# Kernel tuning notes

Hardware: AMD Instinct MI355X
Metric: run time of the kernel (lower is better)

## Reference

```python
import jax, jax.numpy as jnp
import numpy as np
from jax import lax

B, P = 32, 1024          # batch, max_phonemes
V, E, H = 100, 512, 512  # vocab, embedding_dim, hidden_dim
EPS = 1e-5


def setup_inputs() -> dict:
    key = jax.random.key(0)
    ks = jax.random.split(key, 12)
    return {
        "phoneme_ids": jax.random.randint(ks[0], (B, P), 0, V),
        "phoneme_durations": jax.random.randint(ks[1], (B, P), 0, 10),
        "emb": jax.random.normal(ks[2], (V, E), jnp.float32) * 0.02,
        "conv1_w": jax.random.normal(ks[3], (H, E, 3), jnp.float32) * 0.02,
        "conv1_b": jnp.zeros((H,), jnp.float32),
        "bn1_gamma": 1.0 + 0.1 * jax.random.normal(ks[4], (H,), jnp.float32),
        "bn1_beta": 0.1 * jax.random.normal(ks[5], (H,), jnp.float32),
        "bn1_mean": jnp.zeros((H,), jnp.float32),
        "bn1_var": jnp.ones((H,), jnp.float32),
        "conv2_w": jax.random.normal(ks[6], (H, H, 3), jnp.float32) * 0.02,
        "conv2_b": jnp.zeros((H,), jnp.float32),
        "bn2_gamma": 1.0 + 0.1 * jax.random.normal(ks[7], (H,), jnp.float32),
        "bn2_beta": 0.1 * jax.random.normal(ks[8], (H,), jnp.float32),
        "bn2_mean": jnp.zeros((H,), jnp.float32),
        "bn2_var": jnp.ones((H,), jnp.float32),
    }


def _conv_bn_relu(x, w, b, gamma, beta, mean, var):
    # x: [B, C, P]; w: [O, C, 3]; 'same' padding conv1d, inference batchnorm, relu
    y = lax.conv_general_dilated(x, w, (1,), [(1, 1)],
                                 dimension_numbers=("NCH", "OIH", "NCH"))
    y = y + b[None, :, None]
    scale = gamma * lax.rsqrt(var + EPS)
    y = y * scale[None, :, None] + (beta - mean * scale)[None, :, None]
    return jax.nn.relu(y)


def _upsample(x, durations):
    # x: [B, H, P], durations: [B, P] int -> [B, H, max_frames]
    cum = jnp.cumsum(durations, axis=1)              # [B, P]
    total = cum[:, -1]                               # [B]
    max_frames = int(jnp.max(total))                 # concrete (data-derived shape)
    frames = jnp.arange(max_frames)                  # [F]
    # frame f belongs to phoneme p iff cum[p-1] <= f < cum[p]
    idx = jax.vmap(lambda c: jnp.searchsorted(c, frames, side="right"))(cum)
    idx = jnp.minimum(idx, P - 1)                    # [B, F]
    gathered = jnp.take_along_axis(x, idx[:, None, :], axis=2)  # [B, H, F]
    mask = (frames[None, :] < total[:, None]).astype(x.dtype)   # [B, F]
    return gathered * mask[:, None, :]


def reference(phoneme_ids, phoneme_durations, emb,
              conv1_w, conv1_b, bn1_gamma, bn1_beta, bn1_mean, bn1_var,
              conv2_w, conv2_b, bn2_gamma, bn2_beta, bn2_mean, bn2_var):
    x = emb[phoneme_ids]                 # [B, P, E]
    x = jnp.transpose(x, (0, 2, 1))      # [B, E, P]
    x = _conv_bn_relu(x, conv1_w, conv1_b, bn1_gamma, bn1_beta, bn1_mean, bn1_var)
    x = _conv_bn_relu(x, conv2_w, conv2_b, bn2_gamma, bn2_beta, bn2_mean, bn2_var)
    return _upsample(x, phoneme_durations)
```

## Files before the change

### kernel.cpp

```cpp
#include <hip/hip_runtime.h>

#define B_ 32
#define P_ 1024
#define V_ 100
#define E_ 512
#define H_ 512
#define C_ 512
#define EPS_ 1e-5f

typedef float f32x4 __attribute__((ext_vector_type(4)));
typedef short bf16x8 __attribute__((ext_vector_type(8)));

#define GLB(p) ((const __attribute__((address_space(1))) unsigned int*)(p))
#define LDSP(p) ((__attribute__((address_space(3))) unsigned int*)(p))

__device__ __forceinline__ unsigned short f2bf(float f) {
  unsigned int u = __float_as_uint(f);
  u += 0x7fffu + ((u >> 16) & 1u);
  return (unsigned short)(u >> 16);
}
__device__ __forceinline__ float bf2f(unsigned short s) {
  return __uint_as_float(((unsigned int)s) << 16);
}

__global__ void g_kernel(const float* __restrict__ emb, const float* __restrict__ w1,
                         const float* __restrict__ g1, const float* __restrict__ vr1,
                         float* __restrict__ G) {
  __shared__ float se[E_];
  int v = blockIdx.x;
  int h = threadIdx.x;
  se[h] = emb[(size_t)v * E_ + h];
  __syncthreads();
  float a0 = 0.f, a1 = 0.f, a2 = 0.f;
  const float* wrow = w1 + (size_t)h * E_ * 3;
#pragma unroll 4
  for (int e = 0; e < E_; ++e) {
    float x = se[e];
    a0 = fmaf(wrow[e * 3 + 0], x, a0);
    a1 = fmaf(wrow[e * 3 + 1], x, a1);
    a2 = fmaf(wrow[e * 3 + 2], x, a2);
  }
  float sc = g1[h] * rsqrtf(vr1[h] + EPS_);
  G[((size_t)0 * V_ + v) * H_ + h] = a0 * sc;
  G[((size_t)1 * V_ + v) * H_ + h] = a1 * sc;
  G[((size_t)2 * V_ + v) * H_ + h] = a2 * sc;
}

__global__ void a2_kernel(const float* __restrict__ w2,
                          const float* __restrict__ b1, const float* __restrict__ g1,
                          const float* __restrict__ be1, const float* __restrict__ mn1,
                          const float* __restrict__ vr1,
                          const float* __restrict__ b2, const float* __restrict__ g2,
                          const float* __restrict__ be2, const float* __restrict__ mn2,
                          const float* __restrict__ vr2,
                          float* __restrict__ bias1, float* __restrict__ bias2,
                          unsigned short* __restrict__ A2h, unsigned short* __restrict__ A2l) {
  int h = blockIdx.x;
  int tid = threadIdx.x;
  float sc1 = g1[h] * rsqrtf(vr1[h] + EPS_);
  float sc2 = g2[h] * rsqrtf(vr2[h] + EPS_);
  if (tid == 0) {
    bias1[h] = b1[h] * sc1 + be1[h] - mn1[h] * sc1;
    bias2[h] = b2[h] * sc2 + be2[h] - mn2[h] * sc2;
  }
  for (int j = tid; j < 3 * C_; j += 256) {
    int k = j >> 9;
    int c = j & (C_ - 1);
    float val = w2[((size_t)h * C_ + c) * 3 + k] * sc2;
    unsigned short hi = f2bf(val);
    A2h[(size_t)h * (3 * C_) + j] = hi;
    A2l[(size_t)h * (3 * C_) + j] = f2bf(val - bf2f(hi));
  }
}

__global__ void embed_conv1_kernel(const int* __restrict__ ids, const float* __restrict__ G,
                                   const float* __restrict__ bias1,
                                   unsigned short* __restrict__ Bh, unsigned short* __restrict__ Bl) {
  int r = blockIdx.x % (P_ + 2);
  int b = blockIdx.x / (P_ + 2);
  int tid = threadIdx.x;
  size_t outbase = ((size_t)b * (P_ + 2) + r) * C_;
  if (r == 0 || r == P_ + 1) {
    for (int c = tid; c < C_; c += 256) { Bh[outbase + c] = 0; Bl[outbase + c] = 0; }
    return;
  }
  int p = r - 1;
  int v0 = (p >= 1) ? ids[b * P_ + p - 1] : -1;
  int v1 = ids[b * P_ + p];
  int v2 = (p + 1 < P_) ? ids[b * P_ + p + 1] : -1;
  const float* G0 = (v0 >= 0) ? (G + ((size_t)0 * V_ + v0) * H_) : nullptr;
  const float* G1 = G + ((size_t)1 * V_ + v1) * H_;
  const float* G2 = (v2 >= 0) ? (G + ((size_t)2 * V_ + v2) * H_) : nullptr;
  for (int c = tid; c < C_; c += 256) {
    float s = bias1[c] + G1[c];
    if (G0) s += G0[c];
    if (G2) s += G2[c];
    s = fmaxf(s, 0.f);
    unsigned short hi = f2bf(s);
    Bh[outbase + c] = hi;
    Bl[outbase + c] = f2bf(s - bf2f(hi));
  }
}

__global__ void cumsum_kernel(const int* __restrict__ dur, int* __restrict__ cum) {
  __shared__ int s[P_];
  int b = blockIdx.x;
  int t = threadIdx.x;
  s[t] = dur[b * P_ + t];
  __syncthreads();
  for (int off = 1; off < P_; off <<= 1) {
    int v = (t >= off) ? s[t - off] : 0;
    __syncthreads();
    s[t] += v;
    __syncthreads();
  }
  cum[b * P_ + t] = s[t];
}

#define BM 128
#define BN 128
#define BK 32
__global__ __launch_bounds__(256) void conv2_gemm_kernel(
    const unsigned short* __restrict__ A2h, const unsigned short* __restrict__ A2l,
    const unsigned short* __restrict__ Bh, const unsigned short* __restrict__ Bl,
    const float* __restrict__ bias2, float* __restrict__ out2) {
  __shared__ __align__(16) unsigned short lds[4][BM * BK];

  int tid = threadIdx.x;
  int w = tid >> 6;
  int l = tid & 63;
  int m0 = blockIdx.y * BM;
  int n0 = blockIdx.x * BN;
  int b = n0 >> 10;
  int p0 = n0 & (P_ - 1);

  const unsigned short* Ah_base = A2h + (size_t)m0 * (3 * C_);
  const unsigned short* Al_base = A2l + (size_t)m0 * (3 * C_);
  const unsigned short* Bh_base = Bh + ((size_t)b * (P_ + 2) + p0) * C_;
  const unsigned short* Bl_base = Bl + ((size_t)b * (P_ + 2) + p0) * C_;

  f32x4 acc[4][4] = {};

  int srow = l >> 2;
  int scol = (l & 3) * 8;
  int fr = l & 15, fq = l >> 4;
  int wr = (w >> 1) * 64, wc = (w & 1) * 64;

  for (int kt = 0; kt < (3 * C_) / BK; ++kt) {
    int kofs = kt * BK;
#pragma unroll
    for (int q = 0; q < 2; ++q) {
      int seg = q * 4 + w;
      int row = seg * 16 + srow;
      int col = kofs + scol;
      __builtin_amdgcn_global_load_lds(GLB(Ah_base + (size_t)row * (3 * C_) + col),
                                       LDSP(&lds[0][seg * 512]), 16, 0, 0);
      __builtin_amdgcn_global_load_lds(GLB(Al_base + (size_t)row * (3 * C_) + col),
                                       LDSP(&lds[1][seg * 512]), 16, 0, 0);
      __builtin_amdgcn_global_load_lds(GLB(Bh_base + (size_t)row * C_ + col),
                                       LDSP(&lds[2][seg * 512]), 16, 0, 0);
      __builtin_amdgcn_global_load_lds(GLB(Bl_base + (size_t)row * C_ + col),
                                       LDSP(&lds[3][seg * 512]), 16, 0, 0);
    }
    __syncthreads();

    bf16x8 ah[4], al[4], bh[4], bl[4];
#pragma unroll
    for (int i = 0; i < 4; ++i) {
      ah[i] = *(const bf16x8*)&lds[0][(wr + i * 16 + fr) * BK + fq * 8];
      al[i] = *(const bf16x8*)&lds[1][(wr + i * 16 + fr) * BK + fq * 8];
    }
#pragma unroll
    for (int j = 0; j < 4; ++j) {
      bh[j] = *(const bf16x8*)&lds[2][(wc + j * 16 + fr) * BK + fq * 8];
      bl[j] = *(const bf16x8*)&lds[3][(wc + j * 16 + fr) * BK + fq * 8];
    }
#pragma unroll
    for (int i = 0; i < 4; ++i)
#pragma unroll
      for (int j = 0; j < 4; ++j) {
        acc[i][j] = __builtin_amdgcn_mfma_f32_16x16x32_bf16(ah[i], bh[j], acc[i][j], 0, 0, 0);
        acc[i][j] = __builtin_amdgcn_mfma_f32_16x16x32_bf16(ah[i], bl[j], acc[i][j], 0, 0, 0);
        acc[i][j] = __builtin_amdgcn_mfma_f32_16x16x32_bf16(al[i], bh[j], acc[i][j], 0, 0, 0);
      }
    __syncthreads();
  }

#pragma unroll
  for (int i = 0; i < 4; ++i) {
#pragma unroll
    for (int j = 0; j < 4; ++j) {
#pragma unroll
      for (int r = 0; r < 4; ++r) {
        int m = m0 + wr + i * 16 + fq * 4 + r;
        int n = n0 + wc + j * 16 + fr;
        int bb = n >> 10;
        int p = n & (P_ - 1);
        float v = acc[i][j][r] + bias2[m];
        v = fmaxf(v, 0.f);
        out2[((size_t)bb * H_ + m) * P_ + p] = v;
      }
    }
  }
}

__global__ void upsample_kernel(const float* __restrict__ out2, const int* __restrict__ cum,
                                float* __restrict__ out, int T) {
  __shared__ int sc[P_];
  int b = blockIdx.y;
  int tid = threadIdx.x;
  for (int i = tid; i < P_; i += 256) sc[i] = cum[b * P_ + i];
  __syncthreads();
  int t = blockIdx.x * 256 + tid;
  if (t >= T) return;
  int tot = sc[P_ - 1];
  bool valid = (t < tot);
  int idx = 0;
  if (valid) {
    int lo = 0, hi = P_;
    while (lo < hi) {
      int mid = (lo + hi) >> 1;
      if (sc[mid] <= t) lo = mid + 1; else hi = mid;
    }
    idx = min(lo, P_ - 1);
  }
  const float* src = out2 + (size_t)b * H_ * P_ + idx;
  float* dst = out + (size_t)b * H_ * T + t;
  if (valid) {
    for (int h = 0; h < H_; ++h) dst[(size_t)h * T] = src[(size_t)h * P_];
  } else {
    for (int h = 0; h < H_; ++h) dst[(size_t)h * T] = 0.f;
  }
}

static inline size_t align256(size_t x) { return (x + 255) & ~(size_t)255; }

extern "C" void kernel_launch(void* const* d_in, const int* in_sizes, int n_in,
                              void* d_out, int out_size, void* d_ws, size_t ws_size,
                              hipStream_t stream) {
  const int*   ids = (const int*)d_in[0];
  const int*   dur = (const int*)d_in[1];
  const float* emb = (const float*)d_in[2];
  const float* w1  = (const float*)d_in[3];
  const float* b1  = (const float*)d_in[4];
  const float* g1  = (const float*)d_in[5];
  const float* be1 = (const float*)d_in[6];
  const float* mn1 = (const float*)d_in[7];
  const float* vr1 = (const float*)d_in[8];
  const float* w2  = (const float*)d_in[9];
  const float* b2  = (const float*)d_in[10];
  const float* g2  = (const float*)d_in[11];
  const float* be2 = (const float*)d_in[12];
  const float* mn2 = (const float*)d_in[13];
  const float* vr2 = (const float*)d_in[14];
  float* out = (float*)d_out;

  int T = out_size / (B_ * H_);

  char* ws = (char*)d_ws;
  size_t off = 0;
  auto carve = [&](size_t bytes) { void* p = ws + off; off = align256(off + bytes); return p; };
  float* G              = (float*)carve((size_t)3 * V_ * H_ * 4);
  float* bias1          = (float*)carve(H_ * 4);
  float* bias2          = (float*)carve(H_ * 4);
  unsigned short* A2h   = (unsigned short*)carve((size_t)H_ * 3 * C_ * 2);
  unsigned short* A2l   = (unsigned short*)carve((size_t)H_ * 3 * C_ * 2);
  unsigned short* Bhv   = (unsigned short*)carve((size_t)B_ * (P_ + 2) * C_ * 2);
  unsigned short* Blv   = (unsigned short*)carve((size_t)B_ * (P_ + 2) * C_ * 2);
  float* out2           = (float*)carve((size_t)B_ * H_ * P_ * 4);
  int* cum              = (int*)carve((size_t)B_ * P_ * 4);

  g_kernel<<<V_, E_, 0, stream>>>(emb, w1, g1, vr1, G);
  a2_kernel<<<H_, 256, 0, stream>>>(w2, b1, g1, be1, mn1, vr1, b2, g2, be2, mn2, vr2,
                                    bias1, bias2, A2h, A2l);
  embed_conv1_kernel<<<B_ * (P_ + 2), 256, 0, stream>>>(ids, G, bias1, Bhv, Blv);
  cumsum_kernel<<<B_, P_, 0, stream>>>(dur, cum);
  conv2_gemm_kernel<<<dim3((B_ * P_) / BN, H_ / BM), 256, 0, stream>>>(A2h, A2l, Bhv, Blv,
                                                                       bias2, out2);
  upsample_kernel<<<dim3((T + 255) / 256, B_), 256, 0, stream>>>(out2, cum, out, T);
}
```

Baseline: 744.3 us.

## Transpose conv1 weights, vectorize embed stores, remap GEMM block order

Adds a tiled transpose of conv1 weights so g_kernel reads coalesced rows, and splits g_kernel across more blocks of 64 threads. embed_conv1 now uses float2 loads and packed 32-bit bf16 stores. The conv2 GEMM grid is flattened and remapped with a swizzle across groups of 8 blocks to change L2 locality. Several launch bounds are added. The costs are an extra kernel launch and a 3 MB workspace buffer.

```diff
diff --git a/kernel.cpp b/kernel.cpp
--- a/kernel.cpp
+++ b/kernel.cpp
@@ -23,22 +23,40 @@
   return __uint_as_float(((unsigned int)s) << 16);
 }
 
-__global__ void g_kernel(const float* __restrict__ emb, const float* __restrict__ w1,
-                         const float* __restrict__ g1, const float* __restrict__ vr1,
-                         float* __restrict__ G) {
+__global__ __launch_bounds__(256) void w1t_kernel(const float* __restrict__ w1,
+                                                  float* __restrict__ w1T) {
+  __shared__ float tile[64][65];
+  int h0 = blockIdx.x * 64;
+  int e0 = blockIdx.y * 64;
+  int t = threadIdx.x;
+  int c = t & 63, r4 = t >> 6;
+#pragma unroll
+  for (int r = 0; r < 64; r += 4)
+    tile[r + r4][c] = w1[(size_t)(h0 + r + r4) * 1536 + e0 + c];
+  __syncthreads();
+#pragma unroll
+  for (int r = 0; r < 64; r += 4)
+    w1T[(size_t)(e0 + r + r4) * 512 + h0 + c] = tile[c][r + r4];
+}
+
+__global__ __launch_bounds__(64) void g_kernel(const float* __restrict__ emb,
+                                               const float* __restrict__ w1T,
+                                               const float* __restrict__ g1,
+                                               const float* __restrict__ vr1,
+                                               float* __restrict__ G) {
   __shared__ float se[E_];
   int v = blockIdx.x;
-  int h = threadIdx.x;
-  se[h] = emb[(size_t)v * E_ + h];
+  int h = blockIdx.y * 64 + threadIdx.x;
+  for (int i = threadIdx.x; i < E_; i += 64) se[i] = emb[(size_t)v * E_ + i];
   __syncthreads();
   float a0 = 0.f, a1 = 0.f, a2 = 0.f;
-  const float* wrow = w1 + (size_t)h * E_ * 3;
 #pragma unroll 4
   for (int e = 0; e < E_; ++e) {
     float x = se[e];
-    a0 = fmaf(wrow[e * 3 + 0], x, a0);
-    a1 = fmaf(wrow[e * 3 + 1], x, a1);
-    a2 = fmaf(wrow[e * 3 + 2], x, a2);
+    const float* wp = w1T + (size_t)(3 * e) * H_ + h;
+    a0 = fmaf(wp[0], x, a0);
+    a1 = fmaf(wp[H_], x, a1);
+    a2 = fmaf(wp[2 * H_], x, a2);
   }
   float sc = g1[h] * rsqrtf(vr1[h] + EPS_);
   G[((size_t)0 * V_ + v) * H_ + h] = a0 * sc;
@@ -46,15 +64,15 @@
   G[((size_t)2 * V_ + v) * H_ + h] = a2 * sc;
 }
 
-__global__ void a2_kernel(const float* __restrict__ w2,
-                          const float* __restrict__ b1, const float* __restrict__ g1,
-                          const float* __restrict__ be1, const float* __restrict__ mn1,
-                          const float* __restrict__ vr1,
-                          const float* __restrict__ b2, const float* __restrict__ g2,
-                          const float* __restrict__ be2, const float* __restrict__ mn2,
-                          const float* __restrict__ vr2,
-                          float* __restrict__ bias1, float* __restrict__ bias2,
-                          unsigned short* __restrict__ A2h, unsigned short* __restrict__ A2l) {
+__global__ __launch_bounds__(256) void a2_kernel(
+    const float* __restrict__ w2, const float* __restrict__ b1,
+    const float* __restrict__ g1, const float* __restrict__ be1,
+    const float* __restrict__ mn1, const float* __restrict__ vr1,
+    const float* __restrict__ b2, const float* __restrict__ g2,
+    const float* __restrict__ be2, const float* __restrict__ mn2,
+    const float* __restrict__ vr2, float* __restrict__ bias1,
+    float* __restrict__ bias2, unsigned short* __restrict__ A2h,
+    unsigned short* __restrict__ A2l) {
   int h = blockIdx.x;
   int tid = threadIdx.x;
   float sc1 = g1[h] * rsqrtf(vr1[h] + EPS_);
@@ -73,36 +91,54 @@
   }
 }
 
-__global__ void embed_conv1_kernel(const int* __restrict__ ids, const float* __restrict__ G,
-                                   const float* __restrict__ bias1,
-                                   unsigned short* __restrict__ Bh, unsigned short* __restrict__ Bl) {
+__global__ __launch_bounds__(256) void embed_conv1_kernel(
+    const int* __restrict__ ids, const float* __restrict__ G,
+    const float* __restrict__ bias1, unsigned short* __restrict__ Bh,
+    unsigned short* __restrict__ Bl) {
   int r = blockIdx.x % (P_ + 2);
   int b = blockIdx.x / (P_ + 2);
-  int tid = threadIdx.x;
+  int t = threadIdx.x;
   size_t outbase = ((size_t)b * (P_ + 2) + r) * C_;
+  unsigned int* BhU = (unsigned int*)(Bh + outbase);
+  unsigned int* BlU = (unsigned int*)(Bl + outbase);
   if (r == 0 || r == P_ + 1) {
-    for (int c = tid; c < C_; c += 256) { Bh[outbase + c] = 0; Bl[outbase + c] = 0; }
+    BhU[t] = 0u;
+    BlU[t] = 0u;
     return;
   }
   int p = r - 1;
   int v0 = (p >= 1) ? ids[b * P_ + p - 1] : -1;
   int v1 = ids[b * P_ + p];
   int v2 = (p + 1 < P_) ? ids[b * P_ + p + 1] : -1;
-  const float* G0 = (v0 >= 0) ? (G + ((size_t)0 * V_ + v0) * H_) : nullptr;
-  const float* G1 = G + ((size_t)1 * V_ + v1) * H_;
-  const float* G2 = (v2 >= 0) ? (G + ((size_t)2 * V_ + v2) * H_) : nullptr;
-  for (int c = tid; c < C_; c += 256) {
-    float s = bias1[c] + G1[c];
-    if (G0) s += G0[c];
-    if (G2) s += G2[c];
-    s = fmaxf(s, 0.f);
-    unsigned short hi = f2bf(s);
-    Bh[outbase + c] = hi;
-    Bl[outbase + c] = f2bf(s - bf2f(hi));
-  }
-}
-
-__global__ void cumsum_kernel(const int* __restrict__ dur, int* __restrict__ cum) {
+  const float2* G0 = (v0 >= 0) ? (const float2*)(G + ((size_t)0 * V_ + v0) * H_) : nullptr;
+  const float2* G1 = (const float2*)(G + ((size_t)1 * V_ + v1) * H_);
+  const float2* G2 = (v2 >= 0) ? (const float2*)(G + ((size_t)2 * V_ + v2) * H_) : nullptr;
+  const float2* bi = (const float2*)bias1;
+
+  float2 s = bi[t];
+  float2 gm = G1[t];
+  s.x += gm.x;
+  s.y += gm.y;
+  if (G0) {
+    float2 g0 = G0[t];
+    s.x += g0.x;
+    s.y += g0.y;
+  }
+  if (G2) {
+    float2 g2v = G2[t];
+    s.x += g2v.x;
+    s.y += g2v.y;
+  }
+  s.x = fmaxf(s.x, 0.f);
+  s.y = fmaxf(s.y, 0.f);
+  unsigned short h0 = f2bf(s.x), h1 = f2bf(s.y);
+  unsigned short l0 = f2bf(s.x - bf2f(h0)), l1 = f2bf(s.y - bf2f(h1));
+  BhU[t] = (unsigned int)h0 | ((unsigned int)h1 << 16);
+  BlU[t] = (unsigned int)l0 | ((unsigned int)l1 << 16);
+}
+
+__global__ __launch_bounds__(1024) void cumsum_kernel(const int* __restrict__ dur,
+                                                      int* __restrict__ cum) {
   __shared__ int s[P_];
   int b = blockIdx.x;
   int t = threadIdx.x;
@@ -129,8 +165,11 @@
   int tid = threadIdx.x;
   int w = tid >> 6;
   int l = tid & 63;
-  int m0 = blockIdx.y * BM;
-  int n0 = blockIdx.x * BN;
+
+  int bid = blockIdx.x;
+  int wg = ((bid & 7) << 7) | (bid >> 3);
+  int m0 = (wg >> 8) * BM;
+  int n0 = (wg & 255) * BN;
   int b = n0 >> 10;
   int p0 = n0 & (P_ - 1);
 
@@ -204,8 +243,9 @@
   }
 }
 
-__global__ void upsample_kernel(const float* __restrict__ out2, const int* __restrict__ cum,
-                                float* __restrict__ out, int T) {
+__global__ __launch_bounds__(256) void upsample_kernel(const float* __restrict__ out2,
+                                                       const int* __restrict__ cum,
+                                                       float* __restrict__ out, int T) {
   __shared__ int sc[P_];
   int b = blockIdx.y;
   int tid = threadIdx.x;
@@ -261,6 +301,7 @@
   size_t off = 0;
   auto carve = [&](size_t bytes) { void* p = ws + off; off = align256(off + bytes); return p; };
   float* G              = (float*)carve((size_t)3 * V_ * H_ * 4);
+  float* w1T            = (float*)carve((size_t)3 * E_ * H_ * 4);
   float* bias1          = (float*)carve(H_ * 4);
   float* bias2          = (float*)carve(H_ * 4);
   unsigned short* A2h   = (unsigned short*)carve((size_t)H_ * 3 * C_ * 2);
@@ -270,12 +311,13 @@
   float* out2           = (float*)carve((size_t)B_ * H_ * P_ * 4);
   int* cum              = (int*)carve((size_t)B_ * P_ * 4);
 
-  g_kernel<<<V_, E_, 0, stream>>>(emb, w1, g1, vr1, G);
+  w1t_kernel<<<dim3(H_ / 64, (3 * E_) / 64), 256, 0, stream>>>(w1, w1T);
   a2_kernel<<<H_, 256, 0, stream>>>(w2, b1, g1, be1, mn1, vr1, b2, g2, be2, mn2, vr2,
                                     bias1, bias2, A2h, A2l);
+  g_kernel<<<dim3(V_, H_ / 64), 64, 0, stream>>>(emb, w1T, g1, vr1, G);
   embed_conv1_kernel<<<B_ * (P_ + 2), 256, 0, stream>>>(ids, G, bias1, Bhv, Blv);
   cumsum_kernel<<<B_, P_, 0, stream>>>(dur, cum);
-  conv2_gemm_kernel<<<dim3((B_ * P_) / BN, H_ / BM), 256, 0, stream>>>(A2h, A2l, Bhv, Blv,
-                                                                       bias2, out2);
+  conv2_gemm_kernel<<<(B_ * P_ / BN) * (H_ / BM), 256, 0, stream>>>(A2h, A2l, Bhv, Blv,
+                                                                    bias2, out2);
   upsample_kernel<<<dim3((T + 255) / 256, B_), 256, 0, stream>>>(out2, cum, out, T);
 }
```

After: 698.3 us. 1.07x faster.
